# Kernel tuning notes

Measured on AMD Instinct MI355X. Metric: run time of the kernel, lower is better.

## Reference

```python
import jax, jax.numpy as jnp
import numpy as np

B = 8
SHAPE = (4, 16, 16)   # latent video shape; S = prod = 1024
S = 1024
AE = 64               # ae_embed_dim
D = 768               # embed_dim
F = 3072              # mlp_dim
H = 12                # num_heads (heads are re-merged before the score matmul!)
L = 12                # num_layers
C = 17                # n_classes
OUT = 1024            # out_dim
EPS = 1e-6
HD = D // H


def setup_inputs() -> dict:
    key = jax.random.key(0)
    ks = iter(jax.random.split(key, 64))

    def p(shape, s=0.02):
        return jax.random.normal(next(ks), shape, jnp.float32) * s

    inp = {
        'x': jax.random.normal(next(ks), (B, *SHAPE, AE), jnp.float32),
        'mask': jnp.tril(jnp.ones((S, S), bool)),  # causal
        'label': jax.nn.one_hot(jax.random.randint(next(ks), (B,), 0, C), C, dtype=jnp.float32),
        'dense_in_w': p((D, AE)), 'dense_in_b': jnp.zeros((D,), jnp.float32),
        'sos': p((D,)),
        # BroadcastPositionBiases: embed_dim=768 split into 3 chunks of 256
        'pos0': p((SHAPE[0], D // 3)), 'pos1': p((SHAPE[1], D // 3)), 'pos2': p((SHAPE[2], D // 3)),
        'ln1_sw': p((L, D, C)), 'ln1_bw': p((L, D, C)),
        'qkv_w': p((L, 3 * D, D)), 'qkv_b': jnp.zeros((L, 3 * D), jnp.float32),
        'ao1_w': p((L, D, D)), 'ao1_b': jnp.zeros((L, D), jnp.float32),  # DotProductAttention.out_proj
        'ao2_w': p((L, D, D)), 'ao2_b': jnp.zeros((L, D), jnp.float32),  # MultiHeadAttention.out_proj
        'ln2_sw': p((L, D, C)), 'ln2_bw': p((L, D, C)),
        'mlp_w1': p((L, F, D)), 'mlp_b1': jnp.zeros((L, F), jnp.float32),
        'mlp_w2': p((L, D, F)), 'mlp_b2': jnp.zeros((L, D), jnp.float32),
        'lnf_sw': p((D, C)), 'lnf_bw': p((D, C)),
        'out_w': p((OUT, D)), 'out_b': jnp.zeros((OUT,), jnp.float32),
    }
    return inp


def cond_ln(x, cond, sw, bw):
    # conditional LayerNorm: mul = rsqrt(var+eps)*(1+Linear(cond)), bias = Linear(cond)
    mean = jnp.mean(x, axis=-1, keepdims=True)
    var = jnp.mean((x - mean) ** 2, axis=-1, keepdims=True)
    scale = cond @ sw.T   # [B, D]
    bias = cond @ bw.T    # [B, D]
    mul = jax.lax.rsqrt(var + EPS) * (1.0 + scale[:, None, :])
    return (x - mean) * mul + bias[:, None, :]


def pos_bias(embs, shape):
    n = len(shape)
    outs = []
    for i, e in enumerate(embs):
        sh = [1] * n + [e.shape[-1]]
        sh[i] = shape[i]
        outs.append(jnp.broadcast_to(e.reshape(sh), tuple(shape) + (e.shape[-1],)))
    return jnp.concatenate(outs, axis=-1).reshape(-1, sum(e.shape[-1] for e in embs))  # [S, D]


def attn_block(h, mask, qkv_w, qkv_b, o1_w, o1_b, o2_w, o2_b):
    Bn, Sn, Dn = h.shape
    qkv = h @ qkv_w.T + qkv_b                       # [B, S, 3D]
    qkv = qkv.reshape(Bn, Sn, H, 3 * HD)            # per-head [q|k|v] layout
    q = qkv[..., :HD].reshape(Bn, Sn, Dn)           # heads re-merged BEFORE scores
    k = qkv[..., HD:2 * HD].reshape(Bn, Sn, Dn)
    v = qkv[..., 2 * HD:].reshape(Bn, Sn, Dn)
    # NOTE: scaling uses full embed_dim (module quirk), not head_dim
    scores = jnp.einsum('bqd,bkd->bqk', q * (float(Dn) ** -0.5), k)
    scores = jnp.where(mask[None, :, :], scores, -jnp.inf)
    w = jax.nn.softmax(scores, axis=-1)
    out = jnp.einsum('bqk,bkd->bqd', w, v)
    out = out @ o1_w.T + o1_b                        # DotProductAttention.out_proj
    out = out @ o2_w.T + o2_b                        # MultiHeadAttention.out_proj (applied twice)
    return out


def _forward(x, mask, label, dense_in_w, dense_in_b, sos, pos0, pos1, pos2,
             ln1_sw, ln1_bw, qkv_w, qkv_b, ao1_w, ao1_b, ao2_w, ao2_b,
             ln2_sw, ln2_bw, mlp_w1, mlp_b1, mlp_w2, mlp_b2,
             lnf_sw, lnf_bw, out_w, out_b):
    Bn = x.shape[0]
    old_shape = x.shape[1:-1]
    h = x.reshape(Bn, -1, x.shape[-1]) @ dense_in_w.T + dense_in_b   # [B, S, D]
    # right shift with learned SOS token
    h = jnp.concatenate([jnp.broadcast_to(sos, (Bn, 1, D)), h[:, :-1]], axis=1)
    pb = pos_bias([pos0, pos1, pos2], old_shape)                     # [S, D]
    h = h + pb[None, :h.shape[1]]
    for l in range(L):
        hn = cond_ln(h, label, ln1_sw[l], ln1_bw[l])
        h = h + attn_block(hn, mask, qkv_w[l], qkv_b[l], ao1_w[l], ao1_b[l], ao2_w[l], ao2_b[l])
        hn = cond_ln(h, label, ln2_sw[l], ln2_bw[l])
        m = hn @ mlp_w1[l].T + mlp_b1[l]
        m = jax.nn.sigmoid(1.702 * m) * m           # GELU2
        m = m @ mlp_w2[l].T + mlp_b2[l]
        h = h + m
    h = cond_ln(h, label, lnf_sw, lnf_bw)
    out = h @ out_w.T + out_b                        # [B, S, OUT]
    return out.reshape(Bn, *old_shape, out.shape[-1])


def reference(x, mask, label, dense_in_w, dense_in_b, sos, pos0, pos1, pos2,
              ln1_sw, ln1_bw, qkv_w, qkv_b, ao1_w, ao1_b, ao2_w, ao2_b,
              ln2_sw, ln2_bw, mlp_w1, mlp_b1, mlp_w2, mlp_b2,
              lnf_sw, lnf_bw, out_w, out_b):
    return _forward(x, mask, label, dense_in_w, dense_in_b, sos, pos0, pos1, pos2,
                    ln1_sw, ln1_bw, qkv_w, qkv_b, ao1_w, ao1_b, ao2_w, ao2_b,
                    ln2_sw, ln2_bw, mlp_w1, mlp_b1, mlp_w2, mlp_b2,
                    lnf_sw, lnf_bw, out_w, out_b)
```

## Files before the change

kernel.cpp:

```cpp
#include <hip/hip_runtime.h>

typedef __bf16 bf16;
typedef __bf16 bf16x8 __attribute__((ext_vector_type(8)));
typedef __bf16 bf16x4 __attribute__((ext_vector_type(4)));
typedef float  f32x4  __attribute__((ext_vector_type(4)));

#define DEV __device__ __forceinline__

DEV void gload_lds16(const bf16* g, bf16* l) {
    __builtin_amdgcn_global_load_lds(
        (__attribute__((address_space(1))) void*)g,
        (__attribute__((address_space(3))) void*)l, 16, 0, 0);
}

enum { M_QKV, M_SCORES, M_PV, M_BIAS, M_RESID, M_GELU, M_OUT };

template<int MODE>
__global__ __launch_bounds__(256)
void gemm_k(const bf16* __restrict__ A, const bf16* __restrict__ B,
            int M, int N, int K,
            long long batchA, long long batchB, long long batchC,
            const float* __restrict__ bias,
            bf16* __restrict__ Cb, float* __restrict__ Cf,
            bf16* __restrict__ qp, bf16* __restrict__ kp, bf16* __restrict__ vp)
{
    const int bm = blockIdx.x, bn = blockIdx.y, bz = blockIdx.z;
    if (MODE == M_SCORES && bn > bm) return;
    int kTiles = K >> 5;
    if (MODE == M_PV) {
        int lim = (bm + 1) * 4;
        if (lim < kTiles) kTiles = lim;
    }

    const int tid = threadIdx.x, wid = tid >> 6, lane = tid & 63;
    const bf16* Ab = A + (long long)bz * batchA + (long long)bm * 128 * K;
    const bf16* Bb = B + (long long)bz * batchB + (long long)bn * 128 * K;

    __shared__ __align__(16) bf16 sA[2][4096];
    __shared__ __align__(16) bf16 sB[2][4096];

    const int srow = wid * 16 + (lane >> 2);
    const int scol = (lane & 3) * 8;
    const long long aoff = (long long)srow * K + scol;

    auto stage = [&](int buf, int kt) {
        const bf16* ga = Ab + (long long)kt * 32;
        const bf16* gb = Bb + (long long)kt * 32;
        gload_lds16(ga + aoff,            &sA[buf][(wid * 16) * 32]);
        gload_lds16(ga + aoff + 64LL * K, &sA[buf][(64 + wid * 16) * 32]);
        gload_lds16(gb + aoff,            &sB[buf][(wid * 16) * 32]);
        gload_lds16(gb + aoff + 64LL * K, &sB[buf][(64 + wid * 16) * 32]);
    };

    f32x4 acc[4][4];
#pragma unroll
    for (int m = 0; m < 4; ++m)
#pragma unroll
        for (int n = 0; n < 4; ++n) acc[m][n] = (f32x4){0.f, 0.f, 0.f, 0.f};

    stage(0, 0);
    __syncthreads();

    const int wr = wid >> 1, wc = wid & 1;
    const int arow = wr * 64 + (lane & 15);
    const int brow = wc * 64 + (lane & 15);
    const int koff = (lane >> 4) * 8;

    for (int kt = 0; kt < kTiles; ++kt) {
        const int cur = kt & 1;
        if (kt + 1 < kTiles) stage(cur ^ 1, kt + 1);
        bf16x8 af[4], bfr[4];
#pragma unroll
        for (int m = 0; m < 4; ++m)
            af[m] = *(const bf16x8*)&sA[cur][(arow + m * 16) * 32 + koff];
#pragma unroll
        for (int n = 0; n < 4; ++n)
            bfr[n] = *(const bf16x8*)&sB[cur][(brow + n * 16) * 32 + koff];
#pragma unroll
        for (int m = 0; m < 4; ++m)
#pragma unroll
            for (int n = 0; n < 4; ++n)
                acc[m][n] = __builtin_amdgcn_mfma_f32_16x16x32_bf16(af[m], bfr[n], acc[m][n], 0, 0, 0);
        __syncthreads();
    }

    const int cr0 = bm * 128 + wr * 64 + (lane >> 4) * 4;
    const int cc0 = bn * 128 + wc * 64 + (lane & 15);
#pragma unroll
    for (int m = 0; m < 4; ++m) {
#pragma unroll
        for (int n = 0; n < 4; ++n) {
            const int col = cc0 + n * 16;
#pragma unroll
            for (int r = 0; r < 4; ++r) {
                const int row = cr0 + m * 16 + r;
                float v = acc[m][n][r];
                if (MODE == M_QKV) {
                    v += bias[col];
                    int hd = col / 192, rr = col % 192;
                    int b = row >> 10, s = row & 1023;
                    if (rr < 64)
                        qp[(long long)row * 768 + hd * 64 + rr] = (bf16)(v * 0.03608439182435161f);
                    else if (rr < 128)
                        kp[(long long)row * 768 + hd * 64 + (rr - 64)] = (bf16)v;
                    else
                        vp[((long long)b * 768 + hd * 64 + (rr - 128)) * 1024 + s] = (bf16)v;
                } else if (MODE == M_SCORES || MODE == M_PV) {
                    Cb[(long long)bz * batchC + (long long)row * N + col] = (bf16)v;
                } else if (MODE == M_BIAS) {
                    Cb[(long long)row * N + col] = (bf16)(v + bias[col]);
                } else if (MODE == M_RESID) {
                    long long idx = (long long)row * N + col;
                    Cf[idx] += v + bias[col];
                } else if (MODE == M_GELU) {
                    float xg = v + bias[col];
                    Cb[(long long)row * N + col] = (bf16)(xg / (1.f + __expf(-1.702f * xg)));
                } else {
                    Cf[(long long)row * N + col] = v + bias[col];
                }
            }
        }
    }
}

__global__ __launch_bounds__(256)
void cvt_bf16_k(const float* __restrict__ in, bf16* __restrict__ out, int n4)
{
    int i = blockIdx.x * 256 + threadIdx.x;
    if (i >= n4) return;
    float4 f = ((const float4*)in)[i];
    bf16x4 o = { (bf16)f.x, (bf16)f.y, (bf16)f.z, (bf16)f.w };
    ((bf16x4*)out)[i] = o;
}

__global__ __launch_bounds__(256)
void cond_proj_k(const float* __restrict__ label, const float* __restrict__ sw,
                 const float* __restrict__ bw, float* __restrict__ scale,
                 float* __restrict__ bias, int total)
{
    int idx = blockIdx.x * 256 + threadIdx.x;
    if (idx >= total) return;
    int l = idx / 6144;
    int rem = idx - l * 6144;
    int b = rem / 768, d = rem - (rem / 768) * 768;
    const float* lab = label + b * 17;
    const float* swp = sw + ((long long)l * 768 + d) * 17;
    const float* bwp = bw + ((long long)l * 768 + d) * 17;
    float s = 0.f, bb = 0.f;
#pragma unroll
    for (int c = 0; c < 17; ++c) { float lv = lab[c]; s += lv * swp[c]; bb += lv * bwp[c]; }
    scale[idx] = s;
    bias[idx]  = bb;
}

__global__ __launch_bounds__(256)
void embed_k(const float* __restrict__ x, const float* __restrict__ w,
             const float* __restrict__ wb, const float* __restrict__ sos,
             const float* __restrict__ p0, const float* __restrict__ p1,
             const float* __restrict__ p2, float* __restrict__ h)
{
    const int s = blockIdx.x, b = blockIdx.y;
    __shared__ __align__(16) float xr[64];
    if (s > 0 && threadIdx.x < 64)
        xr[threadIdx.x] = x[((long long)b * 1024 + (s - 1)) * 64 + threadIdx.x];
    __syncthreads();
    const int i0 = s >> 8, i1 = (s >> 4) & 15, i2 = s & 15;
#pragma unroll
    for (int j = 0; j < 3; ++j) {
        const int d = j * 256 + threadIdx.x;
        float v;
        if (s == 0) {
            v = sos[d];
        } else {
            const float4* wr4 = (const float4*)(w + (long long)d * 64);
            const float4* xr4 = (const float4*)xr;
            float acc = 0.f;
#pragma unroll
            for (int t = 0; t < 16; ++t) {
                float4 wv = wr4[t], xv = xr4[t];
                acc += wv.x * xv.x + wv.y * xv.y + wv.z * xv.z + wv.w * xv.w;
            }
            v = wb[d] + acc;
        }
        float pbv = (d < 256) ? p0[i0 * 256 + d]
                  : (d < 512) ? p1[i1 * 256 + (d - 256)]
                              : p2[i2 * 256 + (d - 512)];
        h[((long long)b * 1024 + s) * 768 + d] = v + pbv;
    }
}

__global__ __launch_bounds__(256)
void cond_ln_k(const float* __restrict__ h, const float* __restrict__ scale,
               const float* __restrict__ bias, bf16* __restrict__ out)
{
    const long long row = (long long)blockIdx.y * 1024 + blockIdx.x;
    const int b = blockIdx.y;
    const float* hr = h + row * 768;
    float v[3], sum = 0.f, sq = 0.f;
#pragma unroll
    for (int j = 0; j < 3; ++j) {
        v[j] = hr[j * 256 + threadIdx.x];
        sum += v[j]; sq += v[j] * v[j];
    }
    __shared__ float sm[8];
#pragma unroll
    for (int o = 32; o; o >>= 1) { sum += __shfl_down(sum, o); sq += __shfl_down(sq, o); }
    const int wid = threadIdx.x >> 6;
    if ((threadIdx.x & 63) == 0) { sm[wid] = sum; sm[4 + wid] = sq; }
    __syncthreads();
    sum = sm[0] + sm[1] + sm[2] + sm[3];
    sq  = sm[4] + sm[5] + sm[6] + sm[7];
    const float mean = sum * (1.f / 768.f);
    const float var  = sq * (1.f / 768.f) - mean * mean;
    const float rs   = rsqrtf(var + 1e-6f);
    const float* sc = scale + (long long)b * 768;
    const float* bi = bias  + (long long)b * 768;
    bf16* orow = out + row * 768;
#pragma unroll
    for (int j = 0; j < 3; ++j) {
        const int d = j * 256 + threadIdx.x;
        orow[d] = (bf16)((v[j] - mean) * rs * (1.f + sc[d]) + bi[d]);
    }
}

__global__ __launch_bounds__(256)
void softmax_k(bf16* __restrict__ P)
{
    const int i = blockIdx.x, b = blockIdx.y;
    bf16* row = P + ((long long)b * 1024 + i) * 1024;
    const int len = i + 1;
    float v[4], mx = -1e30f;
#pragma unroll
    for (int j = 0; j < 4; ++j) {
        int c = j * 256 + threadIdx.x;
        v[j] = (c < len) ? (float)row[c] : -1e30f;
        mx = fmaxf(mx, v[j]);
    }
    __shared__ float sm[8];
#pragma unroll
    for (int o = 32; o; o >>= 1) mx = fmaxf(mx, __shfl_down(mx, o));
    const int wid = threadIdx.x >> 6;
    if ((threadIdx.x & 63) == 0) sm[wid] = mx;
    __syncthreads();
    mx = fmaxf(fmaxf(sm[0], sm[1]), fmaxf(sm[2], sm[3]));
    float s = 0.f;
#pragma unroll
    for (int j = 0; j < 4; ++j) {
        v[j] = __expf(v[j] - mx);
        s += ((j * 256 + threadIdx.x) < len) ? v[j] : 0.f;
    }
#pragma unroll
    for (int o = 32; o; o >>= 1) s += __shfl_down(s, o);
    if ((threadIdx.x & 63) == 0) sm[4 + wid] = s;
    __syncthreads();
    s = sm[4] + sm[5] + sm[6] + sm[7];
    const float inv = 1.f / s;
#pragma unroll
    for (int j = 0; j < 4; ++j) {
        int c = j * 256 + threadIdx.x;
        row[c] = (c < len) ? (bf16)(v[j] * inv) : (bf16)0.f;
    }
}

__global__ __launch_bounds__(256)
void fill_k(float* o, int n, float v)
{
    int i = blockIdx.x * 256 + threadIdx.x;
    if (i < n) o[i] = v;
}

extern "C" void kernel_launch(void* const* d_in, const int* in_sizes, int n_in,
                              void* d_out, int out_size, void* d_ws, size_t ws_size,
                              hipStream_t stream)
{
    (void)in_sizes; (void)n_in;
    const float* x     = (const float*)d_in[0];
    const float* label = (const float*)d_in[2];
    const float* dw    = (const float*)d_in[3];
    const float* db    = (const float*)d_in[4];
    const float* sos   = (const float*)d_in[5];
    const float* p0    = (const float*)d_in[6];
    const float* p1    = (const float*)d_in[7];
    const float* p2    = (const float*)d_in[8];
    const float* ln1sw = (const float*)d_in[9];
    const float* ln1bw = (const float*)d_in[10];
    const float* qkvw  = (const float*)d_in[11];
    const float* qkvb  = (const float*)d_in[12];
    const float* ao1w  = (const float*)d_in[13];
    const float* ao1b  = (const float*)d_in[14];
    const float* ao2w  = (const float*)d_in[15];
    const float* ao2b  = (const float*)d_in[16];
    const float* ln2sw = (const float*)d_in[17];
    const float* ln2bw = (const float*)d_in[18];
    const float* m1w   = (const float*)d_in[19];
    const float* m1b   = (const float*)d_in[20];
    const float* m2w   = (const float*)d_in[21];
    const float* m2b   = (const float*)d_in[22];
    const float* lnfsw = (const float*)d_in[23];
    const float* lnfbw = (const float*)d_in[24];
    const float* outw  = (const float*)d_in[25];
    const float* outb  = (const float*)d_in[26];
    float* out = (float*)d_out;

    char* p = (char*)d_ws;
    auto alloc = [&](size_t bytes) { void* r = (void*)p; p += (bytes + 255) & ~(size_t)255; return r; };
    float* h    = (float*)alloc(8192LL * 768 * 4);
    bf16*  hn   = (bf16*) alloc(8192LL * 768 * 2);
    bf16*  q    = (bf16*) alloc(8192LL * 768 * 2);
    bf16*  kbuf = (bf16*) alloc(8192LL * 768 * 2);
    bf16*  vT   = (bf16*) alloc(8192LL * 768 * 2);
    bf16*  P    = (bf16*) alloc(8LL * 1024 * 1024 * 2);
    bf16*  attn = (bf16*) alloc(8192LL * 768 * 2);
    bf16*  o1o  = (bf16*) alloc(8192LL * 768 * 2);
    bf16*  mb   = (bf16*) alloc(8192LL * 3072 * 2);
    bf16*  wqkv = (bf16*) alloc(2304LL * 768 * 2);
    bf16*  wo1  = (bf16*) alloc(768LL * 768 * 2);
    bf16*  wo2  = (bf16*) alloc(768LL * 768 * 2);
    bf16*  wm1  = (bf16*) alloc(3072LL * 768 * 2);
    bf16*  wm2  = (bf16*) alloc(3072LL * 768 * 2);
    bf16*  wout = (bf16*) alloc(1024LL * 768 * 2);
    float* s1   = (float*)alloc(12LL * 8 * 768 * 4);
    float* b1   = (float*)alloc(12LL * 8 * 768 * 4);
    float* s2   = (float*)alloc(12LL * 8 * 768 * 4);
    float* b2   = (float*)alloc(12LL * 8 * 768 * 4);
    float* sf   = (float*)alloc(8LL * 768 * 4);
    float* bfb  = (float*)alloc(8LL * 768 * 4);

    size_t needed = (size_t)(p - (char*)d_ws);
    if (needed > ws_size) {
        fill_k<<<(out_size + 255) / 256, 256, 0, stream>>>(out, out_size, 1e9f);
        return;
    }

    cvt_bf16_k<<<1024 * 768 / 4 / 256, 256, 0, stream>>>(outw, wout, 1024 * 768 / 4);
    cond_proj_k<<<(12 * 8 * 768 + 255) / 256, 256, 0, stream>>>(label, ln1sw, ln1bw, s1, b1, 12 * 8 * 768);
    cond_proj_k<<<(12 * 8 * 768 + 255) / 256, 256, 0, stream>>>(label, ln2sw, ln2bw, s2, b2, 12 * 8 * 768);
    cond_proj_k<<<(8 * 768 + 255) / 256, 256, 0, stream>>>(label, lnfsw, lnfbw, sf, bfb, 8 * 768);
    embed_k<<<dim3(1024, 8), 256, 0, stream>>>(x, dw, db, sos, p0, p1, p2, h);

    for (int l = 0; l < 12; ++l) {
        cvt_bf16_k<<<2304 * 768 / 4 / 256, 256, 0, stream>>>(qkvw + (long long)l * 2304 * 768, wqkv, 2304 * 768 / 4);
        cvt_bf16_k<<< 768 * 768 / 4 / 256, 256, 0, stream>>>(ao1w + (long long)l * 768 * 768,  wo1,  768 * 768 / 4);
        cvt_bf16_k<<< 768 * 768 / 4 / 256, 256, 0, stream>>>(ao2w + (long long)l * 768 * 768,  wo2,  768 * 768 / 4);
        cvt_bf16_k<<<3072 * 768 / 4 / 256, 256, 0, stream>>>(m1w  + (long long)l * 3072 * 768, wm1,  3072 * 768 / 4);
        cvt_bf16_k<<<3072 * 768 / 4 / 256, 256, 0, stream>>>(m2w  + (long long)l * 768 * 3072, wm2,  3072 * 768 / 4);

        cond_ln_k<<<dim3(1024, 8), 256, 0, stream>>>(h, s1 + (long long)l * 6144, b1 + (long long)l * 6144, hn);

        gemm_k<M_QKV><<<dim3(64, 18, 1), 256, 0, stream>>>(
            hn, wqkv, 8192, 2304, 768, 0, 0, 0,
            qkvb + (long long)l * 2304, nullptr, nullptr, q, kbuf, vT);

        gemm_k<M_SCORES><<<dim3(8, 8, 8), 256, 0, stream>>>(
            q, kbuf, 1024, 1024, 768, 1024LL * 768, 1024LL * 768, 1024LL * 1024,
            nullptr, P, nullptr, nullptr, nullptr, nullptr);

        softmax_k<<<dim3(1024, 8), 256, 0, stream>>>(P);

        gemm_k<M_PV><<<dim3(8, 6, 8), 256, 0, stream>>>(
            P, vT, 1024, 768, 1024, 1024LL * 1024, 768LL * 1024, 1024LL * 768,
            nullptr, attn, nullptr, nullptr, nullptr, nullptr);

        gemm_k<M_BIAS><<<dim3(64, 6, 1), 256, 0, stream>>>(
            attn, wo1, 8192, 768, 768, 0, 0, 0,
            ao1b + (long long)l * 768, o1o, nullptr, nullptr, nullptr, nullptr);

        gemm_k<M_RESID><<<dim3(64, 6, 1), 256, 0, stream>>>(
            o1o, wo2, 8192, 768, 768, 0, 0, 0,
            ao2b + (long long)l * 768, nullptr, h, nullptr, nullptr, nullptr);

        cond_ln_k<<<dim3(1024, 8), 256, 0, stream>>>(h, s2 + (long long)l * 6144, b2 + (long long)l * 6144, hn);

        gemm_k<M_GELU><<<dim3(64, 24, 1), 256, 0, stream>>>(
            hn, wm1, 8192, 3072, 768, 0, 0, 0,
            m1b + (long long)l * 3072, mb, nullptr, nullptr, nullptr, nullptr);

        gemm_k<M_RESID><<<dim3(64, 6, 1), 256, 0, stream>>>(
            mb, wm2, 8192, 768, 3072, 0, 0, 0,
            m2b + (long long)l * 768, nullptr, h, nullptr, nullptr, nullptr);
    }

    cond_ln_k<<<dim3(1024, 8), 256, 0, stream>>>(h, sf, bfb, hn);
    gemm_k<M_OUT><<<dim3(64, 8, 1), 256, 0, stream>>>(
        hn, wout, 8192, 1024, 768, 0, 0, 0,
        outb, nullptr, out, nullptr, nullptr, nullptr);
}
```

Baseline: 4.443 ms.

## Add 64-row GEMM variant for narrow GEMMs, batch weight conversion, MFMA input embedding

```diff
diff --git a/kernel.cpp b/kernel.cpp
--- a/kernel.cpp
+++ b/kernel.cpp
@@ -25,12 +25,7 @@
             bf16* __restrict__ qp, bf16* __restrict__ kp, bf16* __restrict__ vp)
 {
     const int bm = blockIdx.x, bn = blockIdx.y, bz = blockIdx.z;
-    if (MODE == M_SCORES && bn > bm) return;
     int kTiles = K >> 5;
-    if (MODE == M_PV) {
-        int lim = (bm + 1) * 4;
-        if (lim < kTiles) kTiles = lim;
-    }
 
     const int tid = threadIdx.x, wid = tid >> 6, lane = tid & 63;
     const bf16* Ab = A + (long long)bz * batchA + (long long)bm * 128 * K;
@@ -105,16 +100,102 @@
                         kp[(long long)row * 768 + hd * 64 + (rr - 64)] = (bf16)v;
                     else
                         vp[((long long)b * 768 + hd * 64 + (rr - 128)) * 1024 + s] = (bf16)v;
-                } else if (MODE == M_SCORES || MODE == M_PV) {
+                } else if (MODE == M_GELU) {
+                    float xg = v + bias[col];
+                    Cb[(long long)row * N + col] = (bf16)(xg / (1.f + __expf(-1.702f * xg)));
+                } else {
+                    Cf[(long long)row * N + col] = v + bias[col];
+                }
+            }
+        }
+    }
+}
+
+template<int MODE>
+__global__ __launch_bounds__(256)
+void gemm64_k(const bf16* __restrict__ A, const bf16* __restrict__ B,
+              int M, int N, int K,
+              long long batchA, long long batchB, long long batchC,
+              const float* __restrict__ bias,
+              bf16* __restrict__ Cb, float* __restrict__ Cf)
+{
+    const int bm = blockIdx.x, bn = blockIdx.y, bz = blockIdx.z;
+    if (MODE == M_SCORES && 2 * bn > bm) return;
+    int kTiles = K >> 5;
+    if (MODE == M_PV) {
+        int lim = 2 * bm + 2;
+        if (lim < kTiles) kTiles = lim;
+    }
+
+    const int tid = threadIdx.x, wid = tid >> 6, lane = tid & 63;
+    const bf16* Ab = A + (long long)bz * batchA + (long long)bm * 64 * K;
+    const bf16* Bb = B + (long long)bz * batchB + (long long)bn * 128 * K;
+
+    __shared__ __align__(16) bf16 sA[2][2048];
+    __shared__ __align__(16) bf16 sB[2][4096];
+
+    const int srow = wid * 16 + (lane >> 2);
+    const int scol = (lane & 3) * 8;
+    const long long aoff = (long long)srow * K + scol;
+
+    auto stage = [&](int buf, int kt) {
+        const bf16* ga = Ab + (long long)kt * 32;
+        const bf16* gb = Bb + (long long)kt * 32;
+        gload_lds16(ga + aoff,            &sA[buf][(wid * 16) * 32]);
+        gload_lds16(gb + aoff,            &sB[buf][(wid * 16) * 32]);
+        gload_lds16(gb + aoff + 64LL * K, &sB[buf][(64 + wid * 16) * 32]);
+    };
+
+    f32x4 acc[2][4];
+#pragma unroll
+    for (int m = 0; m < 2; ++m)
+#pragma unroll
+        for (int n = 0; n < 4; ++n) acc[m][n] = (f32x4){0.f, 0.f, 0.f, 0.f};
+
+    stage(0, 0);
+    __syncthreads();
+
+    const int wr = wid >> 1, wc = wid & 1;
+    const int arow = wr * 32 + (lane & 15);
+    const int brow = wc * 64 + (lane & 15);
+    const int koff = (lane >> 4) * 8;
+
+    for (int kt = 0; kt < kTiles; ++kt) {
+        const int cur = kt & 1;
+        if (kt + 1 < kTiles) stage(cur ^ 1, kt + 1);
+        bf16x8 af[2], bfr[4];
+#pragma unroll
+        for (int m = 0; m < 2; ++m)
+            af[m] = *(const bf16x8*)&sA[cur][(arow + m * 16) * 32 + koff];
+#pragma unroll
+        for (int n = 0; n < 4; ++n)
+            bfr[n] = *(const bf16x8*)&sB[cur][(brow + n * 16) * 32 + koff];
+#pragma unroll
+        for (int m = 0; m < 2; ++m)
+#pragma unroll
+            for (int n = 0; n < 4; ++n)
+                acc[m][n] = __builtin_amdgcn_mfma_f32_16x16x32_bf16(af[m], bfr[n], acc[m][n], 0, 0, 0);
+        __syncthreads();
+    }
+
+    const int cr0 = bm * 64 + wr * 32 + (lane >> 4) * 4;
+    const int cc0 = bn * 128 + wc * 64 + (lane & 15);
+#pragma unroll
+    for (int m = 0; m < 2; ++m) {
+#pragma unroll
+        for (int n = 0; n < 4; ++n) {
+            const int col = cc0 + n * 16;
+#pragma unroll
+            for (int r = 0; r < 4; ++r) {
+                const int row = cr0 + m * 16 + r;
+                float v = acc[m][n][r];
+                if (MODE == M_SCORES || MODE == M_PV) {
                     Cb[(long long)bz * batchC + (long long)row * N + col] = (bf16)v;
                 } else if (MODE == M_BIAS) {
                     Cb[(long long)row * N + col] = (bf16)(v + bias[col]);
                 } else if (MODE == M_RESID) {
                     long long idx = (long long)row * N + col;
                     Cf[idx] += v + bias[col];
-                } else if (MODE == M_GELU) {
-                    float xg = v + bias[col];
-                    Cb[(long long)row * N + col] = (bf16)(xg / (1.f + __expf(-1.702f * xg)));
                 } else {
                     Cf[(long long)row * N + col] = v + bias[col];
                 }
@@ -154,34 +235,17 @@
 }
 
 __global__ __launch_bounds__(256)
-void embed_k(const float* __restrict__ x, const float* __restrict__ w,
-             const float* __restrict__ wb, const float* __restrict__ sos,
-             const float* __restrict__ p0, const float* __restrict__ p1,
-             const float* __restrict__ p2, float* __restrict__ h)
+void shift_pos_k(const float* __restrict__ xe, const float* __restrict__ sos,
+                 const float* __restrict__ p0, const float* __restrict__ p1,
+                 const float* __restrict__ p2, float* __restrict__ h)
 {
     const int s = blockIdx.x, b = blockIdx.y;
-    __shared__ __align__(16) float xr[64];
-    if (s > 0 && threadIdx.x < 64)
-        xr[threadIdx.x] = x[((long long)b * 1024 + (s - 1)) * 64 + threadIdx.x];
-    __syncthreads();
     const int i0 = s >> 8, i1 = (s >> 4) & 15, i2 = s & 15;
+    const float* xr = xe + ((long long)b * 1024 + (s - 1)) * 768;
 #pragma unroll
     for (int j = 0; j < 3; ++j) {
         const int d = j * 256 + threadIdx.x;
-        float v;
-        if (s == 0) {
-            v = sos[d];
-        } else {
-            const float4* wr4 = (const float4*)(w + (long long)d * 64);
-            const float4* xr4 = (const float4*)xr;
-            float acc = 0.f;
-#pragma unroll
-            for (int t = 0; t < 16; ++t) {
-                float4 wv = wr4[t], xv = xr4[t];
-                acc += wv.x * xv.x + wv.y * xv.y + wv.z * xv.z + wv.w * xv.w;
-            }
-            v = wb[d] + acc;
-        }
+        float v = (s == 0) ? sos[d] : xr[d];
         float pbv = (d < 256) ? p0[i0 * 256 + d]
                   : (d < 512) ? p1[i1 * 256 + (d - 256)]
                               : p2[i2 * 256 + (d - 512)];
@@ -303,6 +367,7 @@
     float* out = (float*)d_out;
 
     char* p = (char*)d_ws;
+    char* pend = (char*)d_ws + ws_size;
     auto alloc = [&](size_t bytes) { void* r = (void*)p; p += (bytes + 255) & ~(size_t)255; return r; };
     float* h    = (float*)alloc(8192LL * 768 * 4);
     bf16*  hn   = (bf16*) alloc(8192LL * 768 * 2);
@@ -313,11 +378,6 @@
     bf16*  attn = (bf16*) alloc(8192LL * 768 * 2);
     bf16*  o1o  = (bf16*) alloc(8192LL * 768 * 2);
     bf16*  mb   = (bf16*) alloc(8192LL * 3072 * 2);
-    bf16*  wqkv = (bf16*) alloc(2304LL * 768 * 2);
-    bf16*  wo1  = (bf16*) alloc(768LL * 768 * 2);
-    bf16*  wo2  = (bf16*) alloc(768LL * 768 * 2);
-    bf16*  wm1  = (bf16*) alloc(3072LL * 768 * 2);
-    bf16*  wm2  = (bf16*) alloc(3072LL * 768 * 2);
     bf16*  wout = (bf16*) alloc(1024LL * 768 * 2);
     float* s1   = (float*)alloc(12LL * 8 * 768 * 4);
     float* b1   = (float*)alloc(12LL * 8 * 768 * 4);
@@ -326,24 +386,70 @@
     float* sf   = (float*)alloc(8LL * 768 * 4);
     float* bfb  = (float*)alloc(8LL * 768 * 4);
 
-    size_t needed = (size_t)(p - (char*)d_ws);
-    if (needed > ws_size) {
+    size_t base_needed = (size_t)(p - (char*)d_ws);
+    if (base_needed + 16LL * 1024 * 1024 > ws_size) {
         fill_k<<<(out_size + 255) / 256, 256, 0, stream>>>(out, out_size, 1e9f);
         return;
     }
+
+    const long long SZ_QKV = 2304LL * 768, SZ_O = 768LL * 768, SZ_M = 3072LL * 768;
+    size_t all_bytes = (size_t)(12 * (SZ_QKV + 2 * SZ_O + 2 * SZ_M)) * 2;
+    bool allw = ((size_t)(p - (char*)d_ws) + all_bytes + 4096 <= ws_size);
+
+    bf16 *wqkvA, *wo1A, *wo2A, *wm1A, *wm2A;
+    if (allw) {
+        wqkvA = (bf16*)alloc(12 * SZ_QKV * 2);
+        wo1A  = (bf16*)alloc(12 * SZ_O * 2);
+        wo2A  = (bf16*)alloc(12 * SZ_O * 2);
+        wm1A  = (bf16*)alloc(12 * SZ_M * 2);
+        wm2A  = (bf16*)alloc(12 * SZ_M * 2);
+    } else {
+        wqkvA = (bf16*)alloc(SZ_QKV * 2);
+        wo1A  = (bf16*)alloc(SZ_O * 2);
+        wo2A  = (bf16*)alloc(SZ_O * 2);
+        wm1A  = (bf16*)alloc(SZ_M * 2);
+        wm2A  = (bf16*)alloc(SZ_M * 2);
+    }
+
+    bf16*  xbf  = (bf16*)P;
+    bf16*  dwbf = (bf16*)(P + 1024 * 1024);
+    float* xe   = (float*)mb;
 
     cvt_bf16_k<<<1024 * 768 / 4 / 256, 256, 0, stream>>>(outw, wout, 1024 * 768 / 4);
     cond_proj_k<<<(12 * 8 * 768 + 255) / 256, 256, 0, stream>>>(label, ln1sw, ln1bw, s1, b1, 12 * 8 * 768);
     cond_proj_k<<<(12 * 8 * 768 + 255) / 256, 256, 0, stream>>>(label, ln2sw, ln2bw, s2, b2, 12 * 8 * 768);
     cond_proj_k<<<(8 * 768 + 255) / 256, 256, 0, stream>>>(label, lnfsw, lnfbw, sf, bfb, 8 * 768);
-    embed_k<<<dim3(1024, 8), 256, 0, stream>>>(x, dw, db, sos, p0, p1, p2, h);
+
+    if (allw) {
+        cvt_bf16_k<<<(int)(12 * SZ_QKV / 4 / 256), 256, 0, stream>>>(qkvw, wqkvA, (int)(12 * SZ_QKV / 4));
+        cvt_bf16_k<<<(int)(12 * SZ_O / 4 / 256),   256, 0, stream>>>(ao1w, wo1A,  (int)(12 * SZ_O / 4));
+        cvt_bf16_k<<<(int)(12 * SZ_O / 4 / 256),   256, 0, stream>>>(ao2w, wo2A,  (int)(12 * SZ_O / 4));
+        cvt_bf16_k<<<(int)(12 * SZ_M / 4 / 256),   256, 0, stream>>>(m1w,  wm1A,  (int)(12 * SZ_M / 4));
+        cvt_bf16_k<<<(int)(12 * SZ_M / 4 / 256),   256, 0, stream>>>(m2w,  wm2A,  (int)(12 * SZ_M / 4));
+    }
+
+    cvt_bf16_k<<<8192 * 64 / 4 / 256, 256, 0, stream>>>(x, xbf, 8192 * 64 / 4);
+    cvt_bf16_k<<<768 * 64 / 4 / 256, 256, 0, stream>>>(dw, dwbf, 768 * 64 / 4);
+    gemm_k<M_OUT><<<dim3(64, 6, 1), 256, 0, stream>>>(
+        xbf, dwbf, 8192, 768, 64, 0, 0, 0, db, nullptr, xe, nullptr, nullptr, nullptr);
+    shift_pos_k<<<dim3(1024, 8), 256, 0, stream>>>(xe, sos, p0, p1, p2, h);
 
     for (int l = 0; l < 12; ++l) {
-        cvt_bf16_k<<<2304 * 768 / 4 / 256, 256, 0, stream>>>(qkvw + (long long)l * 2304 * 768, wqkv, 2304 * 768 / 4);
-        cvt_bf16_k<<< 768 * 768 / 4 / 256, 256, 0, stream>>>(ao1w + (long long)l * 768 * 768,  wo1,  768 * 768 / 4);
-        cvt_bf16_k<<< 768 * 768 / 4 / 256, 256, 0, stream>>>(ao2w + (long long)l * 768 * 768,  wo2,  768 * 768 / 4);
-        cvt_bf16_k<<<3072 * 768 / 4 / 256, 256, 0, stream>>>(m1w  + (long long)l * 3072 * 768, wm1,  3072 * 768 / 4);
-        cvt_bf16_k<<<3072 * 768 / 4 / 256, 256, 0, stream>>>(m2w  + (long long)l * 768 * 3072, wm2,  3072 * 768 / 4);
+        bf16 *wqkv, *wo1, *wo2, *wm1, *wm2;
+        if (allw) {
+            wqkv = wqkvA + (long long)l * SZ_QKV;
+            wo1  = wo1A  + (long long)l * SZ_O;
+            wo2  = wo2A  + (long long)l * SZ_O;
+            wm1  = wm1A  + (long long)l * SZ_M;
+            wm2  = wm2A  + (long long)l * SZ_M;
+        } else {
+            wqkv = wqkvA; wo1 = wo1A; wo2 = wo2A; wm1 = wm1A; wm2 = wm2A;
+            cvt_bf16_k<<<(int)(SZ_QKV / 4 / 256), 256, 0, stream>>>(qkvw + (long long)l * SZ_QKV, wqkv, (int)(SZ_QKV / 4));
+            cvt_bf16_k<<<(int)(SZ_O / 4 / 256),   256, 0, stream>>>(ao1w + (long long)l * SZ_O,   wo1,  (int)(SZ_O / 4));
+            cvt_bf16_k<<<(int)(SZ_O / 4 / 256),   256, 0, stream>>>(ao2w + (long long)l * SZ_O,   wo2,  (int)(SZ_O / 4));
+            cvt_bf16_k<<<(int)(SZ_M / 4 / 256),   256, 0, stream>>>(m1w  + (long long)l * SZ_M,   wm1,  (int)(SZ_M / 4));
+            cvt_bf16_k<<<(int)(SZ_M / 4 / 256),   256, 0, stream>>>(m2w  + (long long)l * SZ_M,   wm2,  (int)(SZ_M / 4));
+        }
 
         cond_ln_k<<<dim3(1024, 8), 256, 0, stream>>>(h, s1 + (long long)l * 6144, b1 + (long long)l * 6144, hn);
 
@@ -351,23 +457,23 @@
             hn, wqkv, 8192, 2304, 768, 0, 0, 0,
             qkvb + (long long)l * 2304, nullptr, nullptr, q, kbuf, vT);
 
-        gemm_k<M_SCORES><<<dim3(8, 8, 8), 256, 0, stream>>>(
+        gemm64_k<M_SCORES><<<dim3(16, 8, 8), 256, 0, stream>>>(
             q, kbuf, 1024, 1024, 768, 1024LL * 768, 1024LL * 768, 1024LL * 1024,
-            nullptr, P, nullptr, nullptr, nullptr, nullptr);
+            nullptr, P, nullptr);
 
         softmax_k<<<dim3(1024, 8), 256, 0, stream>>>(P);
 
-        gemm_k<M_PV><<<dim3(8, 6, 8), 256, 0, stream>>>(
+        gemm64_k<M_PV><<<dim3(16, 6, 8), 256, 0, stream>>>(
             P, vT, 1024, 768, 1024, 1024LL * 1024, 768LL * 1024, 1024LL * 768,
-            nullptr, attn, nullptr, nullptr, nullptr, nullptr);
-
-        gemm_k<M_BIAS><<<dim3(64, 6, 1), 256, 0, stream>>>(
+            nullptr, attn, nullptr);
+
+        gemm64_k<M_BIAS><<<dim3(128, 6, 1), 256, 0, stream>>>(
             attn, wo1, 8192, 768, 768, 0, 0, 0,
-            ao1b + (long long)l * 768, o1o, nullptr, nullptr, nullptr, nullptr);
-
-        gemm_k<M_RESID><<<dim3(64, 6, 1), 256, 0, stream>>>(
+            ao1b + (long long)l * 768, o1o, nullptr);
+
+        gemm64_k<M_RESID><<<dim3(128, 6, 1), 256, 0, stream>>>(
             o1o, wo2, 8192, 768, 768, 0, 0, 0,
-            ao2b + (long long)l * 768, nullptr, h, nullptr, nullptr, nullptr);
+            ao2b + (long long)l * 768, nullptr, h);
 
         cond_ln_k<<<dim3(1024, 8), 256, 0, stream>>>(h, s2 + (long long)l * 6144, b2 + (long long)l * 6144, hn);
 
@@ -375,13 +481,13 @@
             hn, wm1, 8192, 3072, 768, 0, 0, 0,
             m1b + (long long)l * 3072, mb, nullptr, nullptr, nullptr, nullptr);
 
-        gemm_k<M_RESID><<<dim3(64, 6, 1), 256, 0, stream>>>(
+        gemm64_k<M_RESID><<<dim3(128, 6, 1), 256, 0, stream>>>(
             mb, wm2, 8192, 768, 3072, 0, 0, 0,
-            m2b + (long long)l * 768, nullptr, h, nullptr, nullptr, nullptr);
+            m2b + (long long)l * 768, nullptr, h);
     }
 
     cond_ln_k<<<dim3(1024, 8), 256, 0, stream>>>(h, sf, bfb, hn);
-    gemm_k<M_OUT><<<dim3(64, 8, 1), 256, 0, stream>>>(
+    gemm64_k<M_OUT><<<dim3(128, 8, 1), 256, 0, stream>>>(
         hn, wout, 8192, 1024, 768, 0, 0, 0,
-        outb, nullptr, out, nullptr, nullptr, nullptr);
-}
+        outb, nullptr, out);
+}
```

After: 4.476 ms. Within noise of the previous version (+0.8%).
